# Kernel optimization log

Measured on AMD Instinct MI355X. Metric: run time of the kernel, lower is better.

Reference implementation:

```python
import jax, jax.numpy as jnp
import numpy as np

B, T, P, V, D, DINO, H, L = 32, 40, 256, 4096, 256, 384, 4, 2
HD = D // H          # head dim 64
DFF = 4 * D          # 1024
EPS = 1e-5


def setup_inputs() -> dict:
    key = jax.random.key(0)
    ks = iter(jax.random.split(key, 40))
    rn = lambda shape, s=0.02: jax.random.normal(next(ks), shape, jnp.float32) * s
    return dict(
        patches=jax.random.normal(next(ks), (B, P, DINO), jnp.float32),
        tokens=jax.random.randint(next(ks), (B, T), 0, V, jnp.int32),
        tok_emb=rn((V, D)),
        pos_emb=rn((1, T, D)),
        qkv_w=rn((L, 3 * D, D)), qkv_b=jnp.zeros((L, 3 * D), jnp.float32),
        out_w=rn((L, D, D)), out_b=jnp.zeros((L, D), jnp.float32),
        ln1_s=jnp.ones((L, D), jnp.float32), ln1_b=jnp.zeros((L, D), jnp.float32),
        w1=rn((L, DFF, D)), b1=jnp.zeros((L, DFF), jnp.float32),
        w2=rn((L, D, DFF)), b2=jnp.zeros((L, D), jnp.float32),
        ln2_s=jnp.ones((L, D), jnp.float32), ln2_b=jnp.zeros((L, D), jnp.float32),
        fus_w1=rn((D, DINO + D)), fus_b1=jnp.zeros((D,), jnp.float32),
        fus_w2=rn((D, D)), fus_b2=jnp.zeros((D,), jnp.float32),
        cls_w=rn((V, D)), cls_b=jnp.zeros((V,), jnp.float32),
    )


def _ln(x, s, b):
    m = jnp.mean(x, -1, keepdims=True)
    v = jnp.var(x, -1, keepdims=True)
    return (x - m) * jax.lax.rsqrt(v + EPS) * s + b


def _token_encoder(tokens, tok_emb, pos_emb, qkv_w, qkv_b, out_w, out_b,
                   ln1_s, ln1_b, w1, b1, w2, b2, ln2_s, ln2_b):
    # Causal full-sequence pass: output at position t equals re-running the
    # unmasked encoder on tokens[:, :t+1] and taking the last position.
    x = tok_emb[tokens] + pos_emb[:, :tokens.shape[1], :]   # [B,T,D]
    causal = jnp.triu(jnp.full((T, T), -1e9, jnp.float32), 1)  # [T,T]
    for l in range(L):  # fixed small layer count
        qkv = x @ qkv_w[l].T + qkv_b[l]                     # [B,T,3D]
        q, k, v = jnp.split(qkv, 3, axis=-1)
        q = q.reshape(B, T, H, HD).transpose(0, 2, 1, 3)    # [B,H,T,hd]
        k = k.reshape(B, T, H, HD).transpose(0, 2, 1, 3)
        v = v.reshape(B, T, H, HD).transpose(0, 2, 1, 3)
        scores = jnp.einsum('bhqd,bhkd->bhqk', q, k) / np.sqrt(HD).astype(np.float32)
        attn = jax.nn.softmax(scores + causal, axis=-1)
        ctx = jnp.einsum('bhqk,bhkd->bhqd', attn, v)        # [B,H,T,hd]
        ctx = ctx.transpose(0, 2, 1, 3).reshape(B, T, D)
        x = _ln(x + ctx @ out_w[l].T + out_b[l], ln1_s[l], ln1_b[l])
        h = jax.nn.relu(x @ w1[l].T + b1[l]) @ w2[l].T + b2[l]
        x = _ln(x + h, ln2_s[l], ln2_b[l])
    return x  # [B,T,D]


def reference(patches, tokens, tok_emb, pos_emb, qkv_w, qkv_b, out_w, out_b,
              ln1_s, ln1_b, w1, b1, w2, b2, ln2_s, ln2_b,
              fus_w1, fus_b1, fus_w2, fus_b2, cls_w, cls_b):
    enc = _token_encoder(tokens, tok_emb, pos_emb, qkv_w, qkv_b, out_w, out_b,
                         ln1_s, ln1_b, w1, b1, w2, b2, ln2_s, ln2_b)  # [B,T,D]
    # context for step 0 is zeros; step t>0 uses encoder output at position t-1
    ctx = jnp.concatenate([jnp.zeros((B, 1, D), enc.dtype), enc[:, :-1]], axis=1)  # [B,T,D]
    # fusion MLP: split the concat-linear into a patch part and a context part
    wp, wc = fus_w1[:, :DINO], fus_w1[:, DINO:]
    pproj = patches @ wp.T                                  # [B,P,D]
    cproj = ctx @ wc.T + fus_b1                             # [B,T,D]
    h = jax.nn.gelu(pproj[:, None, :, :] + cproj[:, :, None, :], approximate=False)  # [B,T,P,D]
    fused = h @ fus_w2.T + fus_b2                           # [B,T,P,D]
    # sigmoid+gather of the 4096-way logits == gather classifier rows, dot, sigmoid
    w_sel = cls_w[tokens]                                   # [B,T,D]
    b_sel = cls_b[tokens]                                   # [B,T]
    logits = jnp.einsum('btpd,btd->btp', fused, w_sel) + b_sel[:, :, None]
    probs = jax.nn.sigmoid(logits)                          # [B,T,P]
    return probs.transpose(0, 2, 1)                         # [B,P,T] == [B,256,40]
```

## Files before the change

### kernel.cpp

```cpp
#include <hip/hip_runtime.h>
#include <hip/hip_bf16.h>

#define B_ 32
#define T_ 40
#define P_ 256
#define V_ 4096
#define D_ 256
#define DINO_ 384
#define H_ 4
#define L_ 2
#define HD_ 64
#define DFF_ 1024
#define EPS_ 1e-5f

typedef __bf16 bf16;
typedef __bf16 bf16x8 __attribute__((ext_vector_type(8)));
typedef float f32x4 __attribute__((ext_vector_type(4)));

#define OFF_QKV 0
#define OFF_OUTW 393216
#define OFF_W1 524288
#define OFF_W2 1048576
#define OFF_FUS 1572864
#define WB_TOTAL 1736704
#define CONV_BLOCKS 848
#define PAT_BLOCKS 1536

__device__ __forceinline__ bf16x8 cvt8(const float* p) {
  float4 f0 = *(const float4*)p;
  float4 f1 = *(const float4*)(p + 4);
  bf16x8 v;
  v[0] = (bf16)f0.x; v[1] = (bf16)f0.y; v[2] = (bf16)f0.z; v[3] = (bf16)f0.w;
  v[4] = (bf16)f1.x; v[5] = (bf16)f1.y; v[6] = (bf16)f1.z; v[7] = (bf16)f1.w;
  return v;
}

__global__ __launch_bounds__(256) void prep_k(
    const int* __restrict__ tokens, const float* __restrict__ tok_emb,
    const float* __restrict__ pos_emb, float* __restrict__ x,
    const float* __restrict__ fus_w2, bf16* __restrict__ w2Tb,
    const float* __restrict__ qkv_w, const float* __restrict__ out_w,
    const float* __restrict__ w1, const float* __restrict__ w2,
    const float* __restrict__ fus_w1, bf16* __restrict__ wb,
    const float* __restrict__ patches, bf16* __restrict__ patb) {
  __shared__ float tile[32][33];
  int bi = blockIdx.x;
  int tid = threadIdx.x;
  if (bi < B_ * T_) {
    int t = bi % T_;
    x[bi * D_ + tid] = tok_emb[tokens[bi] * D_ + tid] + pos_emb[t * D_ + tid];
  } else if (bi < B_ * T_ + 64) {
    int tt = bi - B_ * T_;
    int bx = (tt & 7) * 32, by = (tt >> 3) * 32;
    int tx = tid & 31, ty = tid >> 5;
#pragma unroll
    for (int i = 0; i < 32; i += 8) tile[ty + i][tx] = fus_w2[(by + ty + i) * D_ + bx + tx];
    __syncthreads();
#pragma unroll
    for (int i = 0; i < 32; i += 8)
      w2Tb[(bx + ty + i) * D_ + by + tx] = (bf16)tile[tx][ty + i];
  } else if (bi < B_ * T_ + 64 + CONV_BLOCKS) {
    long f = (long)(bi - B_ * T_ - 64) * 2048 + tid * 8;
    const float* src;
    long off;
    if (f < OFF_OUTW)      { src = qkv_w;  off = f - OFF_QKV; }
    else if (f < OFF_W1)   { src = out_w;  off = f - OFF_OUTW; }
    else if (f < OFF_W2)   { src = w1;     off = f - OFF_W1; }
    else if (f < OFF_FUS)  { src = w2;     off = f - OFF_W2; }
    else                   { src = fus_w1; off = f - OFF_FUS; }
    *(bf16x8*)&wb[f] = cvt8(src + off);
  } else {
    long f = (long)(bi - B_ * T_ - 64 - CONV_BLOCKS) * 2048 + tid * 8;
    *(bf16x8*)&patb[f] = cvt8(patches + f);
  }
}

template <int ABF16, int OBF16, int RELU, int RESID>
__global__ __launch_bounds__(256) void gemm_k(
    const void* __restrict__ Av, const bf16* __restrict__ W,
    const float* __restrict__ bias, const float* __restrict__ resid,
    void* __restrict__ outv, int K, int lda, int ldw, int ldc) {
  __shared__ bf16 As[32 * 72];
  __shared__ bf16 Ws[32 * 72];
  const int tid = threadIdx.x;
  const int lane = tid & 63;
  const int wv = tid >> 6;
  const int mi = wv & 1, ni = wv >> 1;
  const int col = lane & 15, quad = lane >> 4;
  const int bn = blockIdx.x * 32, bm = blockIdx.y * 32;
  const int srow = tid >> 3, kc = (tid & 7) * 8;
  const float* Af = (const float*)Av;
  const bf16* Ab = (const bf16*)Av;
  const bf16* Wp = W + (long)(bn + srow) * ldw + kc;

  f32x4 acc = {0.f, 0.f, 0.f, 0.f};
  for (int kk = 0; kk < K; kk += 64) {
    if (ABF16)
      *(bf16x8*)&As[srow * 72 + kc] = *(const bf16x8*)(Ab + (long)(bm + srow) * lda + kk + kc);
    else
      *(bf16x8*)&As[srow * 72 + kc] = cvt8(Af + (long)(bm + srow) * lda + kk + kc);
    *(bf16x8*)&Ws[srow * 72 + kc] = *(const bf16x8*)(Wp + kk);
    __syncthreads();
#pragma unroll
    for (int ki = 0; ki < 2; ++ki) {
      bf16x8 afr = *(const bf16x8*)&As[(mi * 16 + col) * 72 + ki * 32 + quad * 8];
      bf16x8 bfr = *(const bf16x8*)&Ws[(ni * 16 + col) * 72 + ki * 32 + quad * 8];
      acc = __builtin_amdgcn_mfma_f32_16x16x32_bf16(afr, bfr, acc, 0, 0, 0);
    }
    __syncthreads();
  }
  const int n = bn + ni * 16 + col;
  float bv = bias ? bias[n] : 0.0f;
#pragma unroll
  for (int r = 0; r < 4; ++r) {
    int m = bm + mi * 16 + quad * 4 + r;
    float val = acc[r] + bv;
    if (RESID) val += resid[(long)m * D_ + n];
    if (RELU) val = fmaxf(val, 0.0f);
    if (OBF16) ((bf16*)outv)[(long)m * ldc + n] = (bf16)val;
    else ((float*)outv)[(long)m * ldc + n] = val;
  }
}

__global__ __launch_bounds__(256) void ln_k(const float* __restrict__ s,
                                            float* __restrict__ xout,
                                            const float* __restrict__ g,
                                            const float* __restrict__ be) {
  int wv = threadIdx.x >> 6, lane = threadIdx.x & 63;
  int m = blockIdx.x * 4 + wv;
  float4 v = *(const float4*)(s + (long)m * D_ + lane * 4);
  float sum = v.x + v.y + v.z + v.w;
  float ss = v.x * v.x + v.y * v.y + v.z * v.z + v.w * v.w;
#pragma unroll
  for (int mk = 1; mk < 64; mk <<= 1) {
    sum += __shfl_xor(sum, mk);
    ss += __shfl_xor(ss, mk);
  }
  float mean = sum * (1.0f / D_);
  float inv = rsqrtf(ss * (1.0f / D_) - mean * mean + EPS_);
  float4 g4 = *(const float4*)(g + lane * 4);
  float4 b4 = *(const float4*)(be + lane * 4);
  float4 o;
  o.x = (v.x - mean) * inv * g4.x + b4.x;
  o.y = (v.y - mean) * inv * g4.y + b4.y;
  o.z = (v.z - mean) * inv * g4.z + b4.z;
  o.w = (v.w - mean) * inv * g4.w + b4.w;
  *(float4*)(xout + (long)m * D_ + lane * 4) = o;
}

__global__ __launch_bounds__(256) void attn_k(const float* __restrict__ qkv,
                                              float* __restrict__ ctx) {
  __shared__ float q[20][HD_ + 1];
  __shared__ float k[T_][HD_ + 1];
  __shared__ float v[T_][HD_ + 1];
  __shared__ float s[20][T_ + 1];
  int h = blockIdx.x, b = blockIdx.y, zq = blockIdx.z;
  int r0 = zq * 20;
  int tid = threadIdx.x;
  int lane = tid & 63, wv = tid >> 6;
  for (int idx = tid; idx < T_ * HD_; idx += 256) {
    int t = idx >> 6, d = idx & 63;
    long base = (long)(b * T_ + t) * (3 * D_) + h * HD_ + d;
    k[t][d] = qkv[base + D_];
    v[t][d] = qkv[base + 2 * D_];
    if (t < 20) q[t][d] = qkv[(long)(b * T_ + r0 + t) * (3 * D_) + h * HD_ + d];
  }
  __syncthreads();
  for (int idx = tid; idx < 20 * T_; idx += 256) {
    int i = idx / T_, j = idx - i * T_;
    if (j <= r0 + i) {
      float acc = 0.f;
#pragma unroll
      for (int d = 0; d < HD_; ++d) acc += q[i][d] * k[j][d];
      s[i][j] = acc * 0.125f;
    }
  }
  __syncthreads();
  for (int rr = wv; rr < 20; rr += 4) {
    int hi = r0 + rr;
    float val = (lane <= hi) ? s[rr][lane] : -1e30f;
    float mx = val;
#pragma unroll
    for (int mk = 1; mk < 64; mk <<= 1) mx = fmaxf(mx, __shfl_xor(mx, mk));
    float e = (lane <= hi)
                  ? __builtin_amdgcn_exp2f((val - mx) * 1.4426950408889634f)
                  : 0.f;
    float sum = e;
#pragma unroll
    for (int mk = 1; mk < 64; mk <<= 1) sum += __shfl_xor(sum, mk);
    float inv = __builtin_amdgcn_rcpf(sum);
    if (lane < T_) s[rr][lane] = e * inv;
  }
  __syncthreads();
  for (int idx = tid; idx < 20 * HD_; idx += 256) {
    int i = idx >> 6, d = idx & 63;
    int hi = r0 + i;
    float acc = 0.f;
    for (int j = 0; j <= hi; ++j) acc += s[i][j] * v[j][d];
    ctx[(long)(b * T_ + hi) * D_ + h * HD_ + d] = acc;
  }
}

__global__ __launch_bounds__(256) void fuse3_k(
    const bf16* __restrict__ patb, const float* __restrict__ sbuf,
    const float* __restrict__ lng, const float* __restrict__ lnb,
    const float* __restrict__ cls_w, const bf16* __restrict__ fusb,
    const bf16* __restrict__ w2Tb, const float* __restrict__ fus_b1,
    const int* __restrict__ tokens, float* __restrict__ pprojT,
    float* __restrict__ cw) {
  __shared__ bf16 As[32 * 264];
  __shared__ bf16 Ws[32 * 72];
  const int tid = threadIdx.x;
  const int lane = tid & 63;
  const int wv = tid >> 6;
  const int mi = wv & 1, ni = wv >> 1;
  const int col = lane & 15, quad = lane >> 4;
  const int bn = blockIdx.x * 32;
  const int y = blockIdx.y;
  const int srow = tid >> 3, kc = (tid & 7) * 8;

  int job, bm, bb = 0;
  if (y < 256) { job = 0; bb = y >> 3; bm = (y & 7) * 32; }
  else if (y < 296) { job = 1; bm = (y - 256) * 32; }
  else { job = 2; bm = (y - 296) * 32; }
  const int gm = bm + srow;

  f32x4 acc = {0.f, 0.f, 0.f, 0.f};
  bf16x8 z8 = {};

  if (job == 1) {
    const int r = srow, cg = (tid & 7) * 32;
    const int t = gm % T_;
    if (t == 0) {
#pragma unroll
      for (int i = 0; i < 4; ++i) *(bf16x8*)&As[r * 264 + cg + i * 8] = z8;
    } else {
      const float* sp = sbuf + (long)(gm - 1) * D_ + cg;
      float v[32];
      float sum = 0.f, ss = 0.f;
#pragma unroll
      for (int i = 0; i < 8; ++i) {
        float4 f = *(const float4*)(sp + i * 4);
        v[i*4] = f.x; v[i*4+1] = f.y; v[i*4+2] = f.z; v[i*4+3] = f.w;
        sum += f.x + f.y + f.z + f.w;
        ss += f.x*f.x + f.y*f.y + f.z*f.z + f.w*f.w;
      }
#pragma unroll
      for (int mk = 1; mk < 8; mk <<= 1) {
        sum += __shfl_xor(sum, mk);
        ss += __shfl_xor(ss, mk);
      }
      float mean = sum * (1.0f / D_);
      float inv = rsqrtf(ss * (1.0f / D_) - mean * mean + EPS_);
#pragma unroll
      for (int i = 0; i < 8; ++i) {
        float4 g4 = *(const float4*)(lng + cg + i * 4);
        float4 b4 = *(const float4*)(lnb + cg + i * 4);
        As[r*264 + cg + i*4]     = (bf16)((v[i*4]   - mean) * inv * g4.x + b4.x);
        As[r*264 + cg + i*4 + 1] = (bf16)((v[i*4+1] - mean) * inv * g4.y + b4.y);
        As[r*264 + cg + i*4 + 2] = (bf16)((v[i*4+2] - mean) * inv * g4.z + b4.z);
        As[r*264 + cg + i*4 + 3] = (bf16)((v[i*4+3] - mean) * inv * g4.w + b4.w);
      }
    }
    __syncthreads();
    const bf16* Wp = fusb + 384 + (long)(bn + srow) * 640 + kc;
    for (int kk = 0; kk < 256; kk += 64) {
      *(bf16x8*)&Ws[srow * 72 + kc] = *(const bf16x8*)(Wp + kk);
      __syncthreads();
#pragma unroll
      for (int ki = 0; ki < 2; ++ki) {
        bf16x8 afr = *(const bf16x8*)&As[(mi*16 + col) * 264 + kk + ki*32 + quad*8];
        bf16x8 bfr = *(const bf16x8*)&Ws[(ni*16 + col) * 72 + ki*32 + quad*8];
        acc = __builtin_amdgcn_mfma_f32_16x16x32_bf16(afr, bfr, acc, 0, 0, 0);
      }
      __syncthreads();
    }
  } else {
    const bf16* Apb;
    const bf16* Wp;
    int K;
    bool gathF = false;
    const float* Apf = nullptr;
    if (job == 0) {
      Apb = fusb + (long)gm * 640;
      Wp = patb + ((long)bb * P_ + bn + srow) * DINO_ + kc;
      K = DINO_;
    } else {
      gathF = true;
      Apf = cls_w + (long)tokens[gm] * D_;
      Wp = w2Tb + (long)(bn + srow) * D_ + kc;
      K = D_;
      Apb = nullptr;
    }
    for (int kk = 0; kk < K; kk += 64) {
      bf16x8 av;
      if (gathF) av = cvt8(Apf + kk + kc);
      else av = *(const bf16x8*)(Apb + kk + kc);
      *(bf16x8*)&As[srow * 72 + kc] = av;
      *(bf16x8*)&Ws[srow * 72 + kc] = *(const bf16x8*)(Wp + kk);
      __syncthreads();
#pragma unroll
      for (int ki = 0; ki < 2; ++ki) {
        bf16x8 afr = *(const bf16x8*)&As[(mi * 16 + col) * 72 + ki * 32 + quad * 8];
        bf16x8 bfr = *(const bf16x8*)&Ws[(ni * 16 + col) * 72 + ki * 32 + quad * 8];
        acc = __builtin_amdgcn_mfma_f32_16x16x32_bf16(afr, bfr, acc, 0, 0, 0);
      }
      __syncthreads();
    }
  }

  const int n = bn + ni * 16 + col;
  if (job == 0) {
#pragma unroll
    for (int r4 = 0; r4 < 4; ++r4) {
      int e = bm + mi * 16 + quad * 4 + r4;
      pprojT[(long)bb * (D_ * P_) + (long)e * P_ + n] = acc[r4];
    }
  } else if (job == 1) {
    float bv = fus_b1[n];
#pragma unroll
    for (int r4 = 0; r4 < 4; ++r4) {
      int m = bm + mi * 16 + quad * 4 + r4;
      cw[(long)m * (2 * D_) + n * 2] = acc[r4] + bv;
    }
  } else {
#pragma unroll
    for (int r4 = 0; r4 < 4; ++r4) {
      int m = bm + mi * 16 + quad * 4 + r4;
      cw[(long)m * (2 * D_) + n * 2 + 1] = acc[r4];
    }
  }
}

__global__ __launch_bounds__(256) void final_k(const float* __restrict__ pprojT,
                                               const float* __restrict__ cw,
                                               const int* __restrict__ tokens,
                                               const float* __restrict__ cls_w,
                                               const float* __restrict__ cls_b,
                                               const float* __restrict__ fus_b2,
                                               float* __restrict__ out) {
  __shared__ float2 cws[4][D_];
  int tid = threadIdx.x;
  int lane = tid & 63, wv = tid >> 6;
  int p = blockIdx.x * 64 + lane;
  int t = blockIdx.y * 4 + wv;
  int b = blockIdx.z;
  int mbase = b * T_ + blockIdx.y * 4;
  for (int idx = tid; idx < 4 * D_; idx += 256) {
    int tt = idx >> 8, e = idx & 255;
    cws[tt][e] = ((const float2*)cw)[(long)(mbase + tt) * D_ + e];
  }
  __syncthreads();

  int m = b * T_ + t;
  int tok = tokens[m];
  const float* cr = cls_w + (long)tok * D_;
  float bacc = 0.f;
#pragma unroll
  for (int i = 0; i < 4; ++i) bacc += cr[lane + i * 64] * fus_b2[lane + i * 64];
#pragma unroll
  for (int mk = 1; mk < 64; mk <<= 1) bacc += __shfl_xor(bacc, mk);
  float beff = bacc + cls_b[tok];

  const float* ppb = pprojT + (long)b * (D_ * P_);
  float acc = 0.f;
#pragma unroll 8
  for (int e = 0; e < D_; ++e) {
    float pp = ppb[e * P_ + p];
    float2 c = cws[wv][e];
    float x = pp + c.x;
    float ex = __builtin_amdgcn_exp2f(-2.4554248f * x);
    float r = __builtin_amdgcn_rcpf(1.0f + ex);
    acc = fmaf(x * r, c.y, acc);
  }
  float logit = acc + beff;
  float es = __builtin_amdgcn_exp2f(-1.4426950408889634f * logit);
  out[(long)(b * P_ + p) * T_ + t] = __builtin_amdgcn_rcpf(1.0f + es);
}

extern "C" void kernel_launch(void* const* d_in, const int* in_sizes, int n_in, void* d_out,
                              int out_size, void* d_ws, size_t ws_size, hipStream_t stream) {
  const float* patches = (const float*)d_in[0];
  const int* tokens = (const int*)d_in[1];
  const float* tok_emb = (const float*)d_in[2];
  const float* pos_emb = (const float*)d_in[3];
  const float* qkv_w = (const float*)d_in[4];
  const float* qkv_b = (const float*)d_in[5];
  const float* out_w = (const float*)d_in[6];
  const float* out_b = (const float*)d_in[7];
  const float* ln1_s = (const float*)d_in[8];
  const float* ln1_b = (const float*)d_in[9];
  const float* w1 = (const float*)d_in[10];
  const float* b1 = (const float*)d_in[11];
  const float* w2 = (const float*)d_in[12];
  const float* b2 = (const float*)d_in[13];
  const float* ln2_s = (const float*)d_in[14];
  const float* ln2_b = (const float*)d_in[15];
  const float* fus_w1 = (const float*)d_in[16];
  const float* fus_b1 = (const float*)d_in[17];
  const float* fus_w2 = (const float*)d_in[18];
  const float* fus_b2 = (const float*)d_in[19];
  const float* cls_w = (const float*)d_in[20];
  const float* cls_b = (const float*)d_in[21];
  float* out = (float*)d_out;

  const int MT = B_ * T_;
  float* x = (float*)d_ws;
  float* qkvbuf = x + MT * D_;
  float* attbuf = qkvbuf + MT * 3 * D_;
  float* s = attbuf + MT * D_;
  float* pprojT = s + MT * D_;
  float* cwbuf = pprojT + (long)B_ * D_ * P_;
  bf16* wb = (bf16*)(cwbuf + MT * D_ * 2);
  bf16* w2Tb = wb + WB_TOTAL;
  bf16* patb = w2Tb + D_ * D_;
  bf16* hb = patb + (long)B_ * P_ * DINO_;

  prep_k<<<MT + 64 + CONV_BLOCKS + PAT_BLOCKS, 256, 0, stream>>>(
      tokens, tok_emb, pos_emb, x, fus_w2, w2Tb, qkv_w, out_w, w1, w2, fus_w1, wb,
      patches, patb);

  for (int l = 0; l < L_; ++l) {
    gemm_k<0, 0, 0, 0><<<dim3(24, 40), 256, 0, stream>>>(
        x, wb + OFF_QKV + (long)l * 3 * D_ * D_, qkv_b + l * 3 * D_, nullptr, qkvbuf,
        D_, D_, D_, 3 * D_);
    attn_k<<<dim3(H_, B_, 2), 256, 0, stream>>>(qkvbuf, attbuf);
    gemm_k<0, 0, 0, 1><<<dim3(8, 40), 256, 0, stream>>>(
        attbuf, wb + OFF_OUTW + (long)l * D_ * D_, out_b + l * D_, x, s, D_, D_, D_, D_);
    ln_k<<<MT / 4, 256, 0, stream>>>(s, x, ln1_s + l * D_, ln1_b + l * D_);
    gemm_k<0, 1, 1, 0><<<dim3(32, 40), 256, 0, stream>>>(
        x, wb + OFF_W1 + (long)l * DFF_ * D_, b1 + l * DFF_, nullptr, hb, D_, D_, D_, DFF_);
    gemm_k<1, 0, 0, 1><<<dim3(8, 40), 256, 0, stream>>>(
        hb, wb + OFF_W2 + (long)l * D_ * DFF_, b2 + l * D_, x, s, DFF_, DFF_, DFF_, D_);
    if (l == 0) ln_k<<<MT / 4, 256, 0, stream>>>(s, x, ln2_s + l * D_, ln2_b + l * D_);
  }

  fuse3_k<<<dim3(8, 336), 256, 0, stream>>>(patb, s, ln2_s + D_, ln2_b + D_, cls_w,
                                            wb + OFF_FUS, w2Tb, fus_b1, tokens,
                                            pprojT, cwbuf);

  final_k<<<dim3(4, 10, 32), 256, 0, stream>>>(pprojT, cwbuf, tokens, cls_w, cls_b,
                                               fus_b2, out);
}
```

Baseline: 245.9 us.

## Fuse layernorm and embedding into GEMM prologues and merge independent stages

Introduces a templated GEMM body that can compute embedding+pos add or layernorm in its A-load prologue, removing separate ln_k and embed passes. The first QKV GEMM now reads the fp32 weights directly inside the prep kernel, the patch projection is co-scheduled with attention, and the classifier-row projection runs alongside the out-proj GEMM. The K loop now stages the whole K (256/384) into shared memory at once instead of 64-wide steps, cutting syncs. This reduces launch count and intermediate traffic, at the cost of larger shared memory per block (lower occupancy) and redundant layernorm work across N-tile blocks.

New measurement: 283.4 us. +15.3%, slower.

```diff
diff --git a/kernel.cpp b/kernel.cpp
--- a/kernel.cpp
+++ b/kernel.cpp
@@ -35,32 +35,199 @@
   return v;
 }
 
-__global__ __launch_bounds__(256) void prep_k(
+template <int ASRC, int KP, int WF32, int OBF16, int RELU, int RESID, int CW>
+__device__ __forceinline__ void gemm_body(
+    bf16* As, bf16* Ws, const void* Av, const void* Wv, const float* bias,
+    const float* resid, const float* aux0, const float* aux1,
+    const int* tokens, float* xout, void* outv, int K, int lda, int ldw,
+    int ldc, int bm, int bn) {
+  const int LDP = KP + 8;
+  const int tid = threadIdx.x;
+  const int lane = tid & 63;
+  const int wv = tid >> 6;
+  const int mi = wv & 1, ni = wv >> 1;
+  const int col = lane & 15, quad = lane >> 4;
+  const int srow = tid >> 3, kc = (tid & 7) * 8;
+  const int gm = bm + srow;
+  f32x4 acc = {0.f, 0.f, 0.f, 0.f};
+
+  if (ASRC == 2 || ASRC == 4) {
+    const int cg = (tid & 7) * 32;
+    bool zero = false;
+    long srcrow = gm;
+    if (ASRC == 4) {
+      if (gm % T_ == 0) zero = true;
+      srcrow = gm - 1;
+    }
+    if (zero) {
+      bf16x8 z8 = {};
+#pragma unroll
+      for (int i = 0; i < 4; ++i) *(bf16x8*)&As[srow * LDP + cg + i * 8] = z8;
+    } else {
+      const float* sp = (const float*)Av + srcrow * D_ + cg;
+      float v[32];
+      float sum = 0.f, ss = 0.f;
+#pragma unroll
+      for (int i = 0; i < 8; ++i) {
+        float4 f = *(const float4*)(sp + i * 4);
+        v[i * 4] = f.x; v[i * 4 + 1] = f.y; v[i * 4 + 2] = f.z; v[i * 4 + 3] = f.w;
+        sum += f.x + f.y + f.z + f.w;
+        ss += f.x * f.x + f.y * f.y + f.z * f.z + f.w * f.w;
+      }
+#pragma unroll
+      for (int mk = 1; mk < 8; mk <<= 1) {
+        sum += __shfl_xor(sum, mk);
+        ss += __shfl_xor(ss, mk);
+      }
+      float mean = sum * (1.0f / D_);
+      float inv = rsqrtf(ss * (1.0f / D_) - mean * mean + EPS_);
+#pragma unroll
+      for (int i = 0; i < 32; ++i) {
+        float o = (v[i] - mean) * inv * aux0[cg + i] + aux1[cg + i];
+        As[srow * LDP + cg + i] = (bf16)o;
+        v[i] = o;
+      }
+      if (ASRC == 2 && xout) {
+#pragma unroll
+        for (int i = 0; i < 8; ++i)
+          *(float4*)(xout + (long)gm * D_ + cg + i * 4) =
+              make_float4(v[i * 4], v[i * 4 + 1], v[i * 4 + 2], v[i * 4 + 3]);
+      }
+    }
+  } else if (ASRC == 5) {
+    const int tok = tokens[gm];
+    const float* te = (const float*)Av + (long)tok * D_;
+    const float* pe = aux0 + (gm % T_) * D_;
+#pragma unroll
+    for (int c = 0; c < KP / 64; ++c) {
+      int off = kc + 64 * c;
+      float4 e0 = *(const float4*)(te + off), e1 = *(const float4*)(te + off + 4);
+      float4 p0 = *(const float4*)(pe + off), p1 = *(const float4*)(pe + off + 4);
+      float o0 = e0.x + p0.x, o1 = e0.y + p0.y, o2 = e0.z + p0.z, o3 = e0.w + p0.w;
+      float o4 = e1.x + p1.x, o5 = e1.y + p1.y, o6 = e1.z + p1.z, o7 = e1.w + p1.w;
+      bf16x8 vv;
+      vv[0] = (bf16)o0; vv[1] = (bf16)o1; vv[2] = (bf16)o2; vv[3] = (bf16)o3;
+      vv[4] = (bf16)o4; vv[5] = (bf16)o5; vv[6] = (bf16)o6; vv[7] = (bf16)o7;
+      *(bf16x8*)&As[srow * LDP + off] = vv;
+      if (xout) {
+        *(float4*)(xout + (long)gm * D_ + off) = make_float4(o0, o1, o2, o3);
+        *(float4*)(xout + (long)gm * D_ + off + 4) = make_float4(o4, o5, o6, o7);
+      }
+    }
+  }
+
+  const float* Af = (const float*)Av;
+  const bf16* Ab = (const bf16*)Av;
+  const float* Wf = (const float*)Wv;
+  const bf16* Wb = (const bf16*)Wv;
+
+  for (int kk0 = 0; kk0 < K; kk0 += KP) {
+    if (ASRC == 0) {
+#pragma unroll
+      for (int c = 0; c < KP / 64; ++c)
+        *(bf16x8*)&As[srow * LDP + kc + 64 * c] =
+            cvt8(Af + (long)gm * lda + kk0 + kc + 64 * c);
+    } else if (ASRC == 1) {
+#pragma unroll
+      for (int c = 0; c < KP / 64; ++c)
+        *(bf16x8*)&As[srow * LDP + kc + 64 * c] =
+            *(const bf16x8*)(Ab + (long)gm * lda + kk0 + kc + 64 * c);
+    } else if (ASRC == 3) {
+      const float* Ag = Af + (long)tokens[gm] * D_;
+#pragma unroll
+      for (int c = 0; c < KP / 64; ++c)
+        *(bf16x8*)&As[srow * LDP + kc + 64 * c] = cvt8(Ag + kk0 + kc + 64 * c);
+    }
+    if (WF32) {
+#pragma unroll
+      for (int c = 0; c < KP / 64; ++c)
+        *(bf16x8*)&Ws[srow * LDP + kc + 64 * c] =
+            cvt8(Wf + (long)(bn + srow) * ldw + kk0 + kc + 64 * c);
+    } else {
+#pragma unroll
+      for (int c = 0; c < KP / 64; ++c)
+        *(bf16x8*)&Ws[srow * LDP + kc + 64 * c] =
+            *(const bf16x8*)(Wb + (long)(bn + srow) * ldw + kk0 + kc + 64 * c);
+    }
+    __syncthreads();
+#pragma unroll
+    for (int ki = 0; ki < KP / 32; ++ki) {
+      bf16x8 afr = *(const bf16x8*)&As[(mi * 16 + col) * LDP + ki * 32 + quad * 8];
+      bf16x8 bfr = *(const bf16x8*)&Ws[(ni * 16 + col) * LDP + ki * 32 + quad * 8];
+      acc = __builtin_amdgcn_mfma_f32_16x16x32_bf16(afr, bfr, acc, 0, 0, 0);
+    }
+    if (kk0 + KP < K) __syncthreads();
+  }
+
+  const int n = bn + ni * 16 + col;
+  float bv = bias ? bias[n] : 0.0f;
+#pragma unroll
+  for (int r = 0; r < 4; ++r) {
+    int m = bm + mi * 16 + quad * 4 + r;
+    float val = acc[r] + bv;
+    if (RESID) val += resid[(long)m * D_ + n];
+    if (RELU) val = fmaxf(val, 0.0f);
+    if (CW == 1) ((float*)outv)[(long)m * (2 * D_) + n * 2] = val;
+    else if (CW == 2) ((float*)outv)[(long)m * (2 * D_) + n * 2 + 1] = val;
+    else if (OBF16) ((bf16*)outv)[(long)m * ldc + n] = (bf16)val;
+    else ((float*)outv)[(long)m * ldc + n] = val;
+  }
+}
+
+struct AttnSM { float q[20][65]; float k[40][65]; float v[40][65]; float s[20][41]; };
+struct Gemm384SM { bf16 As[32 * 392]; bf16 Ws[32 * 392]; };
+struct Gemm256SM { bf16 As[32 * 264]; bf16 Ws[32 * 264]; };
+struct PrepSM { float tile[32][33]; };
+union __align__(16) APSM { AttnSM a; Gemm384SM g; };
+union __align__(16) PQSM { PrepSM p; Gemm256SM g; };
+
+template <int ASRC, int OBF16, int RELU, int RESID, int XW, int CW>
+__global__ __launch_bounds__(256) void gemm_k(
+    const void* __restrict__ Av, const void* __restrict__ Wv,
+    const float* __restrict__ bias, const float* __restrict__ resid,
+    const float* __restrict__ aux0, const float* __restrict__ aux1,
+    const int* __restrict__ tokens, float* __restrict__ xw,
+    void* __restrict__ outv, int K, int lda, int ldw, int ldc) {
+  __shared__ Gemm256SM sm;
+  gemm_body<ASRC, 256, 0, OBF16, RELU, RESID, CW>(
+      sm.As, sm.Ws, Av, Wv, bias, resid, aux0, aux1, tokens,
+      (XW && blockIdx.x == 0) ? xw : nullptr, outv, K, lda, ldw, ldc,
+      blockIdx.y * 32, blockIdx.x * 32);
+}
+
+__global__ __launch_bounds__(256) void pq_k(
     const int* __restrict__ tokens, const float* __restrict__ tok_emb,
     const float* __restrict__ pos_emb, float* __restrict__ x,
     const float* __restrict__ fus_w2, bf16* __restrict__ w2Tb,
     const float* __restrict__ qkv_w, const float* __restrict__ out_w,
     const float* __restrict__ w1, const float* __restrict__ w2,
     const float* __restrict__ fus_w1, bf16* __restrict__ wb,
-    const float* __restrict__ patches, bf16* __restrict__ patb) {
-  __shared__ float tile[32][33];
-  int bi = blockIdx.x;
+    const float* __restrict__ patches, bf16* __restrict__ patb,
+    const float* __restrict__ qkv_b, float* __restrict__ qkvbuf) {
+  __shared__ PQSM sm;
+  int bid = blockIdx.x;
   int tid = threadIdx.x;
-  if (bi < B_ * T_) {
-    int t = bi % T_;
-    x[bi * D_ + tid] = tok_emb[tokens[bi] * D_ + tid] + pos_emb[t * D_ + tid];
-  } else if (bi < B_ * T_ + 64) {
-    int tt = bi - B_ * T_;
-    int bx = (tt & 7) * 32, by = (tt >> 3) * 32;
+  if (bid < 960) {
+    int bnb = bid % 24;
+    gemm_body<5, 256, 1, 0, 0, 0, 0>(
+        sm.g.As, sm.g.Ws, tok_emb, qkv_w, qkv_b, nullptr, pos_emb, nullptr,
+        tokens, (bnb == 0) ? x : nullptr, qkvbuf, 256, 256, 256, 3 * D_,
+        (bid / 24) * 32, bnb * 32);
+    return;
+  }
+  int bi = bid - 960;
+  if (bi < 64) {
+    int bx = (bi & 7) * 32, by = (bi >> 3) * 32;
     int tx = tid & 31, ty = tid >> 5;
 #pragma unroll
-    for (int i = 0; i < 32; i += 8) tile[ty + i][tx] = fus_w2[(by + ty + i) * D_ + bx + tx];
+    for (int i = 0; i < 32; i += 8)
+      sm.p.tile[ty + i][tx] = fus_w2[(by + ty + i) * D_ + bx + tx];
     __syncthreads();
 #pragma unroll
     for (int i = 0; i < 32; i += 8)
-      w2Tb[(bx + ty + i) * D_ + by + tx] = (bf16)tile[tx][ty + i];
-  } else if (bi < B_ * T_ + 64 + CONV_BLOCKS) {
-    long f = (long)(bi - B_ * T_ - 64) * 2048 + tid * 8;
+      w2Tb[(bx + ty + i) * D_ + by + tx] = (bf16)sm.p.tile[tx][ty + i];
+  } else if (bi < 64 + CONV_BLOCKS) {
+    long f = (long)(bi - 64) * 2048 + tid * 8;
     const float* src;
     long off;
     if (f < OFF_OUTW)      { src = qkv_w;  off = f - OFF_QKV; }
@@ -70,94 +237,36 @@
     else                   { src = fus_w1; off = f - OFF_FUS; }
     *(bf16x8*)&wb[f] = cvt8(src + off);
   } else {
-    long f = (long)(bi - B_ * T_ - 64 - CONV_BLOCKS) * 2048 + tid * 8;
+    long f = (long)(bi - 64 - CONV_BLOCKS) * 2048 + tid * 8;
     *(bf16x8*)&patb[f] = cvt8(patches + f);
   }
 }
 
-template <int ABF16, int OBF16, int RELU, int RESID>
-__global__ __launch_bounds__(256) void gemm_k(
-    const void* __restrict__ Av, const bf16* __restrict__ W,
-    const float* __restrict__ bias, const float* __restrict__ resid,
-    void* __restrict__ outv, int K, int lda, int ldw, int ldc) {
-  __shared__ bf16 As[32 * 72];
-  __shared__ bf16 Ws[32 * 72];
-  const int tid = threadIdx.x;
-  const int lane = tid & 63;
-  const int wv = tid >> 6;
-  const int mi = wv & 1, ni = wv >> 1;
-  const int col = lane & 15, quad = lane >> 4;
-  const int bn = blockIdx.x * 32, bm = blockIdx.y * 32;
-  const int srow = tid >> 3, kc = (tid & 7) * 8;
-  const float* Af = (const float*)Av;
-  const bf16* Ab = (const bf16*)Av;
-  const bf16* Wp = W + (long)(bn + srow) * ldw + kc;
-
-  f32x4 acc = {0.f, 0.f, 0.f, 0.f};
-  for (int kk = 0; kk < K; kk += 64) {
-    if (ABF16)
-      *(bf16x8*)&As[srow * 72 + kc] = *(const bf16x8*)(Ab + (long)(bm + srow) * lda + kk + kc);
-    else
-      *(bf16x8*)&As[srow * 72 + kc] = cvt8(Af + (long)(bm + srow) * lda + kk + kc);
-    *(bf16x8*)&Ws[srow * 72 + kc] = *(const bf16x8*)(Wp + kk);
-    __syncthreads();
-#pragma unroll
-    for (int ki = 0; ki < 2; ++ki) {
-      bf16x8 afr = *(const bf16x8*)&As[(mi * 16 + col) * 72 + ki * 32 + quad * 8];
-      bf16x8 bfr = *(const bf16x8*)&Ws[(ni * 16 + col) * 72 + ki * 32 + quad * 8];
-      acc = __builtin_amdgcn_mfma_f32_16x16x32_bf16(afr, bfr, acc, 0, 0, 0);
-    }
-    __syncthreads();
-  }
-  const int n = bn + ni * 16 + col;
-  float bv = bias ? bias[n] : 0.0f;
-#pragma unroll
-  for (int r = 0; r < 4; ++r) {
-    int m = bm + mi * 16 + quad * 4 + r;
-    float val = acc[r] + bv;
-    if (RESID) val += resid[(long)m * D_ + n];
-    if (RELU) val = fmaxf(val, 0.0f);
-    if (OBF16) ((bf16*)outv)[(long)m * ldc + n] = (bf16)val;
-    else ((float*)outv)[(long)m * ldc + n] = val;
-  }
-}
-
-__global__ __launch_bounds__(256) void ln_k(const float* __restrict__ s,
-                                            float* __restrict__ xout,
-                                            const float* __restrict__ g,
-                                            const float* __restrict__ be) {
-  int wv = threadIdx.x >> 6, lane = threadIdx.x & 63;
-  int m = blockIdx.x * 4 + wv;
-  float4 v = *(const float4*)(s + (long)m * D_ + lane * 4);
-  float sum = v.x + v.y + v.z + v.w;
-  float ss = v.x * v.x + v.y * v.y + v.z * v.z + v.w * v.w;
-#pragma unroll
-  for (int mk = 1; mk < 64; mk <<= 1) {
-    sum += __shfl_xor(sum, mk);
-    ss += __shfl_xor(ss, mk);
-  }
-  float mean = sum * (1.0f / D_);
-  float inv = rsqrtf(ss * (1.0f / D_) - mean * mean + EPS_);
-  float4 g4 = *(const float4*)(g + lane * 4);
-  float4 b4 = *(const float4*)(be + lane * 4);
-  float4 o;
-  o.x = (v.x - mean) * inv * g4.x + b4.x;
-  o.y = (v.y - mean) * inv * g4.y + b4.y;
-  o.z = (v.z - mean) * inv * g4.z + b4.z;
-  o.w = (v.w - mean) * inv * g4.w + b4.w;
-  *(float4*)(xout + (long)m * D_ + lane * 4) = o;
-}
-
-__global__ __launch_bounds__(256) void attn_k(const float* __restrict__ qkv,
-                                              float* __restrict__ ctx) {
-  __shared__ float q[20][HD_ + 1];
-  __shared__ float k[T_][HD_ + 1];
-  __shared__ float v[T_][HD_ + 1];
-  __shared__ float s[20][T_ + 1];
-  int h = blockIdx.x, b = blockIdx.y, zq = blockIdx.z;
+__global__ __launch_bounds__(256) void attnp_k(
+    const float* __restrict__ qkv, float* __restrict__ ctx,
+    const bf16* __restrict__ patb, const bf16* __restrict__ fusb,
+    float* __restrict__ pprojT) {
+  __shared__ APSM sm;
+  int bid = blockIdx.x;
+  int tid = threadIdx.x;
+  if (bid >= 256) {
+    int g = bid - 256;
+    int bn = (g & 7) * 32;
+    int y = g >> 3;
+    int bb = y >> 3, bm = (y & 7) * 32;
+    gemm_body<1, 384, 0, 0, 0, 0, 0>(
+        sm.g.As, sm.g.Ws, fusb, patb + (long)bb * P_ * DINO_, nullptr, nullptr,
+        nullptr, nullptr, nullptr, nullptr, pprojT + (long)bb * D_ * P_, 384,
+        640, DINO_, P_, bm, bn);
+    return;
+  }
+  int h = bid & 3, b = (bid >> 2) & 31, zq = bid >> 7;
   int r0 = zq * 20;
-  int tid = threadIdx.x;
   int lane = tid & 63, wv = tid >> 6;
+  float (&q)[20][65] = sm.a.q;
+  float (&k)[40][65] = sm.a.k;
+  float (&v)[40][65] = sm.a.v;
+  float (&s)[20][41] = sm.a.s;
   for (int idx = tid; idx < T_ * HD_; idx += 256) {
     int t = idx >> 6, d = idx & 63;
     long base = (long)(b * T_ + t) * (3 * D_) + h * HD_ + d;
@@ -201,135 +310,22 @@
   }
 }
 
-__global__ __launch_bounds__(256) void fuse3_k(
-    const bf16* __restrict__ patb, const float* __restrict__ sbuf,
-    const float* __restrict__ lng, const float* __restrict__ lnb,
-    const float* __restrict__ cls_w, const bf16* __restrict__ fusb,
-    const bf16* __restrict__ w2Tb, const float* __restrict__ fus_b1,
-    const int* __restrict__ tokens, float* __restrict__ pprojT,
+__global__ __launch_bounds__(256) void ow_k(
+    const float* __restrict__ attb, const bf16* __restrict__ Wout,
+    const float* __restrict__ outb, const float* __restrict__ xres,
+    float* __restrict__ sbuf, const float* __restrict__ cls_w,
+    const bf16* __restrict__ w2Tb, const int* __restrict__ tokens,
     float* __restrict__ cw) {
-  __shared__ bf16 As[32 * 264];
-  __shared__ bf16 Ws[32 * 72];
-  const int tid = threadIdx.x;
-  const int lane = tid & 63;
-  const int wv = tid >> 6;
-  const int mi = wv & 1, ni = wv >> 1;
-  const int col = lane & 15, quad = lane >> 4;
-  const int bn = blockIdx.x * 32;
-  const int y = blockIdx.y;
-  const int srow = tid >> 3, kc = (tid & 7) * 8;
-
-  int job, bm, bb = 0;
-  if (y < 256) { job = 0; bb = y >> 3; bm = (y & 7) * 32; }
-  else if (y < 296) { job = 1; bm = (y - 256) * 32; }
-  else { job = 2; bm = (y - 296) * 32; }
-  const int gm = bm + srow;
-
-  f32x4 acc = {0.f, 0.f, 0.f, 0.f};
-  bf16x8 z8 = {};
-
-  if (job == 1) {
-    const int r = srow, cg = (tid & 7) * 32;
-    const int t = gm % T_;
-    if (t == 0) {
-#pragma unroll
-      for (int i = 0; i < 4; ++i) *(bf16x8*)&As[r * 264 + cg + i * 8] = z8;
-    } else {
-      const float* sp = sbuf + (long)(gm - 1) * D_ + cg;
-      float v[32];
-      float sum = 0.f, ss = 0.f;
-#pragma unroll
-      for (int i = 0; i < 8; ++i) {
-        float4 f = *(const float4*)(sp + i * 4);
-        v[i*4] = f.x; v[i*4+1] = f.y; v[i*4+2] = f.z; v[i*4+3] = f.w;
-        sum += f.x + f.y + f.z + f.w;
-        ss += f.x*f.x + f.y*f.y + f.z*f.z + f.w*f.w;
-      }
-#pragma unroll
-      for (int mk = 1; mk < 8; mk <<= 1) {
-        sum += __shfl_xor(sum, mk);
-        ss += __shfl_xor(ss, mk);
-      }
-      float mean = sum * (1.0f / D_);
-      float inv = rsqrtf(ss * (1.0f / D_) - mean * mean + EPS_);
-#pragma unroll
-      for (int i = 0; i < 8; ++i) {
-        float4 g4 = *(const float4*)(lng + cg + i * 4);
-        float4 b4 = *(const float4*)(lnb + cg + i * 4);
-        As[r*264 + cg + i*4]     = (bf16)((v[i*4]   - mean) * inv * g4.x + b4.x);
-        As[r*264 + cg + i*4 + 1] = (bf16)((v[i*4+1] - mean) * inv * g4.y + b4.y);
-        As[r*264 + cg + i*4 + 2] = (bf16)((v[i*4+2] - mean) * inv * g4.z + b4.z);
-        As[r*264 + cg + i*4 + 3] = (bf16)((v[i*4+3] - mean) * inv * g4.w + b4.w);
-      }
-    }
-    __syncthreads();
-    const bf16* Wp = fusb + 384 + (long)(bn + srow) * 640 + kc;
-    for (int kk = 0; kk < 256; kk += 64) {
-      *(bf16x8*)&Ws[srow * 72 + kc] = *(const bf16x8*)(Wp + kk);
-      __syncthreads();
-#pragma unroll
-      for (int ki = 0; ki < 2; ++ki) {
-        bf16x8 afr = *(const bf16x8*)&As[(mi*16 + col) * 264 + kk + ki*32 + quad*8];
-        bf16x8 bfr = *(const bf16x8*)&Ws[(ni*16 + col) * 72 + ki*32 + quad*8];
-        acc = __builtin_amdgcn_mfma_f32_16x16x32_bf16(afr, bfr, acc, 0, 0, 0);
-      }
-      __syncthreads();
-    }
-  } else {
-    const bf16* Apb;
-    const bf16* Wp;
-    int K;
-    bool gathF = false;
-    const float* Apf = nullptr;
-    if (job == 0) {
-      Apb = fusb + (long)gm * 640;
-      Wp = patb + ((long)bb * P_ + bn + srow) * DINO_ + kc;
-      K = DINO_;
-    } else {
-      gathF = true;
-      Apf = cls_w + (long)tokens[gm] * D_;
-      Wp = w2Tb + (long)(bn + srow) * D_ + kc;
-      K = D_;
-      Apb = nullptr;
-    }
-    for (int kk = 0; kk < K; kk += 64) {
-      bf16x8 av;
-      if (gathF) av = cvt8(Apf + kk + kc);
-      else av = *(const bf16x8*)(Apb + kk + kc);
-      *(bf16x8*)&As[srow * 72 + kc] = av;
-      *(bf16x8*)&Ws[srow * 72 + kc] = *(const bf16x8*)(Wp + kk);
-      __syncthreads();
-#pragma unroll
-      for (int ki = 0; ki < 2; ++ki) {
-        bf16x8 afr = *(const bf16x8*)&As[(mi * 16 + col) * 72 + ki * 32 + quad * 8];
-        bf16x8 bfr = *(const bf16x8*)&Ws[(ni * 16 + col) * 72 + ki * 32 + quad * 8];
-        acc = __builtin_amdgcn_mfma_f32_16x16x32_bf16(afr, bfr, acc, 0, 0, 0);
-      }
-      __syncthreads();
-    }
-  }
-
-  const int n = bn + ni * 16 + col;
-  if (job == 0) {
-#pragma unroll
-    for (int r4 = 0; r4 < 4; ++r4) {
-      int e = bm + mi * 16 + quad * 4 + r4;
-      pprojT[(long)bb * (D_ * P_) + (long)e * P_ + n] = acc[r4];
-    }
-  } else if (job == 1) {
-    float bv = fus_b1[n];
-#pragma unroll
-    for (int r4 = 0; r4 < 4; ++r4) {
-      int m = bm + mi * 16 + quad * 4 + r4;
-      cw[(long)m * (2 * D_) + n * 2] = acc[r4] + bv;
-    }
-  } else {
-#pragma unroll
-    for (int r4 = 0; r4 < 4; ++r4) {
-      int m = bm + mi * 16 + quad * 4 + r4;
-      cw[(long)m * (2 * D_) + n * 2 + 1] = acc[r4];
-    }
-  }
+  __shared__ Gemm256SM sm;
+  int y = blockIdx.y;
+  if (y < 40)
+    gemm_body<0, 256, 0, 0, 0, 1, 0>(
+        sm.As, sm.Ws, attb, Wout, outb, xres, nullptr, nullptr, nullptr,
+        nullptr, sbuf, 256, 256, 256, 256, y * 32, blockIdx.x * 32);
+  else
+    gemm_body<3, 256, 0, 0, 0, 0, 2>(
+        sm.As, sm.Ws, cls_w, w2Tb, nullptr, nullptr, nullptr, nullptr, tokens,
+        nullptr, cw, 256, 256, 256, 256, (y - 40) * 32, blockIdx.x * 32);
 }
 
 __global__ __launch_bounds__(256) void final_k(const float* __restrict__ pprojT,
@@ -416,29 +412,40 @@
   bf16* patb = w2Tb + D_ * D_;
   bf16* hb = patb + (long)B_ * P_ * DINO_;
 
-  prep_k<<<MT + 64 + CONV_BLOCKS + PAT_BLOCKS, 256, 0, stream>>>(
-      tokens, tok_emb, pos_emb, x, fus_w2, w2Tb, qkv_w, out_w, w1, w2, fus_w1, wb,
-      patches, patb);
-
-  for (int l = 0; l < L_; ++l) {
-    gemm_k<0, 0, 0, 0><<<dim3(24, 40), 256, 0, stream>>>(
-        x, wb + OFF_QKV + (long)l * 3 * D_ * D_, qkv_b + l * 3 * D_, nullptr, qkvbuf,
-        D_, D_, D_, 3 * D_);
-    attn_k<<<dim3(H_, B_, 2), 256, 0, stream>>>(qkvbuf, attbuf);
-    gemm_k<0, 0, 0, 1><<<dim3(8, 40), 256, 0, stream>>>(
-        attbuf, wb + OFF_OUTW + (long)l * D_ * D_, out_b + l * D_, x, s, D_, D_, D_, D_);
-    ln_k<<<MT / 4, 256, 0, stream>>>(s, x, ln1_s + l * D_, ln1_b + l * D_);
-    gemm_k<0, 1, 1, 0><<<dim3(32, 40), 256, 0, stream>>>(
-        x, wb + OFF_W1 + (long)l * DFF_ * D_, b1 + l * DFF_, nullptr, hb, D_, D_, D_, DFF_);
-    gemm_k<1, 0, 0, 1><<<dim3(8, 40), 256, 0, stream>>>(
-        hb, wb + OFF_W2 + (long)l * D_ * DFF_, b2 + l * D_, x, s, DFF_, DFF_, DFF_, D_);
-    if (l == 0) ln_k<<<MT / 4, 256, 0, stream>>>(s, x, ln2_s + l * D_, ln2_b + l * D_);
-  }
-
-  fuse3_k<<<dim3(8, 336), 256, 0, stream>>>(patb, s, ln2_s + D_, ln2_b + D_, cls_w,
-                                            wb + OFF_FUS, w2Tb, fus_b1, tokens,
-                                            pprojT, cwbuf);
-
-  final_k<<<dim3(4, 10, 32), 256, 0, stream>>>(pprojT, cwbuf, tokens, cls_w, cls_b,
-                                               fus_b2, out);
-}
+  pq_k<<<960 + 64 + CONV_BLOCKS + PAT_BLOCKS, 256, 0, stream>>>(
+      tokens, tok_emb, pos_emb, x, fus_w2, w2Tb, qkv_w, out_w, w1, w2, fus_w1,
+      wb, patches, patb, qkv_b, qkvbuf);
+
+  attnp_k<<<256 + 2048, 256, 0, stream>>>(qkvbuf, attbuf, patb, wb + OFF_FUS,
+                                          pprojT);
+
+  ow_k<<<dim3(8, 80), 256, 0, stream>>>(attbuf, wb + OFF_OUTW, out_b, x, s,
+                                        cls_w, w2Tb, tokens, cwbuf);
+
+  gemm_k<2, 1, 1, 0, 1, 0><<<dim3(32, 40), 256, 0, stream>>>(
+      s, wb + OFF_W1, b1, nullptr, ln1_s, ln1_b, nullptr, x, hb, 256, 256, 256,
+      DFF_);
+  gemm_k<1, 0, 0, 1, 0, 0><<<dim3(8, 40), 256, 0, stream>>>(
+      hb, wb + OFF_W2, b2, x, nullptr, nullptr, nullptr, nullptr, s, DFF_,
+      DFF_, DFF_, D_);
+  gemm_k<2, 0, 0, 0, 1, 0><<<dim3(24, 40), 256, 0, stream>>>(
+      s, wb + OFF_QKV + 3 * D_ * D_, qkv_b + 3 * D_, nullptr, ln2_s, ln2_b,
+      nullptr, x, qkvbuf, 256, 256, 256, 3 * D_);
+  attnp_k<<<256, 256, 0, stream>>>(qkvbuf, attbuf, patb, wb + OFF_FUS, pprojT);
+  gemm_k<0, 0, 0, 1, 0, 0><<<dim3(8, 40), 256, 0, stream>>>(
+      attbuf, wb + OFF_OUTW + D_ * D_, out_b + D_, x, nullptr, nullptr,
+      nullptr, nullptr, s, 256, 256, 256, D_);
+  gemm_k<2, 1, 1, 0, 1, 0><<<dim3(32, 40), 256, 0, stream>>>(
+      s, wb + OFF_W1 + DFF_ * D_, b1 + DFF_, nullptr, ln1_s + D_, ln1_b + D_,
+      nullptr, x, hb, 256, 256, 256, DFF_);
+  gemm_k<1, 0, 0, 1, 0, 0><<<dim3(8, 40), 256, 0, stream>>>(
+      hb, wb + OFF_W2 + D_ * DFF_, b2 + D_, x, nullptr, nullptr, nullptr,
+      nullptr, s, DFF_, DFF_, DFF_, D_);
+
+  gemm_k<4, 0, 0, 0, 0, 1><<<dim3(8, 40), 256, 0, stream>>>(
+      s, wb + OFF_FUS + DINO_, fus_b1, nullptr, ln2_s + D_, ln2_b + D_,
+      nullptr, nullptr, cwbuf, 256, 256, 640, D_);
+
+  final_k<<<dim3(4, 10, 32), 256, 0, stream>>>(pprojT, cwbuf, tokens, cls_w,
+                                               cls_b, fus_b2, out);
+}
```
